# Kernel optimization log

Hardware: AMD Instinct MI355X
Metric: run time of the kernel (lower is better)

## Reference

```python
import jax, jax.numpy as jnp
import numpy as np

B, D_IN = 8192, 4096
H1, H2, LAT = 2048, 1024, 256
NQ, NL = 16, 2


def setup_inputs() -> dict:
    key = jax.random.key(0)
    ks = jax.random.split(key, 16)
    def lin(k, fan_in, fan_out):
        k1, k2 = jax.random.split(k)
        s = 1.0 / np.sqrt(fan_in)
        W = jax.random.uniform(k1, (fan_out, fan_in), jnp.float32, -s, s)
        b = jax.random.uniform(k2, (fan_out,), jnp.float32, -s, s)
        return W, b
    x = jax.random.normal(ks[0], (B, D_IN), jnp.float32)
    We1, be1 = lin(ks[1], D_IN, H1)
    We2, be2 = lin(ks[2], H1, H2)
    We3, be3 = lin(ks[3], H2, LAT)
    P = jax.random.normal(ks[4], (NL, NQ, 3), jnp.float32)  # ansatz params (rx,ry,rz)
    Wd1, bd1 = lin(ks[5], NQ, H2)
    Wd2, bd2 = lin(ks[6], H2, H1)
    Wd3, bd3 = lin(ks[7], H1, D_IN)
    return {"x": x, "We1": We1, "be1": be1, "We2": We2, "be2": be2,
            "We3": We3, "be3": be3, "P": P, "Wd1": Wd1, "bd1": bd1,
            "Wd2": Wd2, "bd2": bd2, "Wd3": Wd3, "bd3": bd3}


def _quantum_block(latent, P):
    """Exact simulation of the per-qubit circuit (all gates single-qubit, so the
    2^n statevector factorizes into per-qubit 2-vectors (a,b) over |0>,|1>).
    latent: (B, LAT), P: (NL, NQ, 3). Returns Z-expectations (B, NQ)."""
    nq = P.shape[1]
    th = latent[:, :nq]  # encoding RY angles, (B, NQ)
    # RY(th)|0> = cos(th/2)|0> + sin(th/2)|1>
    a = jnp.cos(th / 2).astype(jnp.complex64)  # (B, NQ)
    b = jnp.sin(th / 2).astype(jnp.complex64)
    for l in range(P.shape[0]):
        # RX
        t = P[l, :, 0] / 2
        c, s = jnp.cos(t).astype(jnp.complex64), jnp.sin(t).astype(jnp.complex64)
        a, b = c * a - 1j * s * b, -1j * s * a + c * b
        # RY
        t = P[l, :, 1] / 2
        c, s = jnp.cos(t).astype(jnp.complex64), jnp.sin(t).astype(jnp.complex64)
        a, b = c * a - s * b, s * a + c * b
        # RZ
        t = P[l, :, 2] / 2
        ph = jnp.exp(-1j * t.astype(jnp.complex64))
        a, b = a * ph, b * jnp.conj(ph)
    z = (a.real ** 2 + a.imag ** 2) - (b.real ** 2 + b.imag ** 2)
    return z.astype(latent.dtype)


def reference(x, We1, be1, We2, be2, We3, be3, P,
              Wd1, bd1, Wd2, bd2, Wd3, bd3):
    h = jax.nn.relu(x @ We1.T + be1)
    h = jax.nn.relu(h @ We2.T + be2)
    latent = h @ We3.T + be3            # (B, LAT)
    refined = _quantum_block(latent, P)  # (B, NQ)
    h = jax.nn.relu(refined @ Wd1.T + bd1)
    h = jax.nn.relu(h @ Wd2.T + bd2)
    return h @ Wd3.T + bd3              # (B, D_IN)
```

## Files before the change

### kernel.cpp

```cpp
#include <hip/hip_runtime.h>

typedef __attribute__((ext_vector_type(8))) short bf16x8;
typedef __attribute__((ext_vector_type(4))) float f32x4;

__device__ __forceinline__ unsigned short f2bf(float f) {
    union { float f; unsigned int u; } v; v.f = f;
    unsigned int u = v.u;
    unsigned int r = (u + 0x7FFFu + ((u >> 16) & 1u)) >> 16;
    return (unsigned short)r;
}
__device__ __forceinline__ float bf2f(unsigned short b) {
    union { unsigned int u; float f; } v; v.u = ((unsigned int)b) << 16;
    return v.f;
}

#define GL16(g, l)                                                             \
    __builtin_amdgcn_global_load_lds(                                          \
        (__attribute__((address_space(1))) void*)(void*)(g),                   \
        (__attribute__((address_space(3))) void*)(void*)(l), 16, 0, 0)

#define BAR()   __builtin_amdgcn_s_barrier()
#define LGKM0() asm volatile("s_waitcnt lgkmcnt(0)" ::: "memory")

struct Cast5 {
    const float *s0, *s1, *s2, *s3, *s4;
    unsigned short *d0, *d1, *d2, *d3, *d4;
    int n0, n1, n2, n3, total;
};
__global__ void castall(Cast5 a) {
    int stride = gridDim.x * blockDim.x;
    for (int i = blockIdx.x * blockDim.x + threadIdx.x; i < a.total; i += stride) {
        int j = i; const float* s; unsigned short* d;
        if (j < a.n0) { s = a.s0; d = a.d0; }
        else { j -= a.n0;
            if (j < a.n1) { s = a.s1; d = a.d1; }
            else { j -= a.n1;
                if (j < a.n2) { s = a.s2; d = a.d2; }
                else { j -= a.n2;
                    if (j < a.n3) { s = a.s3; d = a.d3; }
                    else { j -= a.n3; s = a.s4; d = a.d4; } } } }
        float4 v = ((const float4*)s)[j];
        ushort4 o;
        o.x = f2bf(v.x); o.y = f2bf(v.y); o.z = f2bf(v.z); o.w = f2bf(v.w);
        ((ushort4*)d)[j] = o;
    }
}


template<int RELU, int OUT_BF16, int MP>
__global__ __launch_bounds__(512, 2) void gemm8p(
    const unsigned short* __restrict__ A,
    const unsigned short* __restrict__ Bm,
    const float* __restrict__ bias,
    void* __restrict__ Cout,
    int N, int K, int NT)
{
    constexpr int AHU  = MP * 2048;
    constexpr int BOFF = MP * 8192;
    __shared__ __align__(16) unsigned short lds[MP * 8192 + 32768];

    const int tid  = threadIdx.x;
    const int lane = tid & 63;
    const int w    = tid >> 6;
    const int wm   = w >> 2;
    const int wn   = w & 3;
    const int bm   = blockIdx.x;
    const int bn   = blockIdx.y;

    const unsigned short* gA = A  + (long)bm * (MP * 64) * K;
    const unsigned short* gB = Bm + (long)bn * 256 * K;

    const int sr0 = tid >> 3;
    const int so0 = (((tid & 7) * 16) ^ ((sr0 & 7) << 4)) >> 1;
    const int loff = (sr0 * K + so0) * 2;
    const int ch1  = K * 128;
    const int lb0 = (w * 64) * 8;
    const int lb1 = (512 + w * 64) * 8;

    const int cl  = lane & 15;
    const int g16 = (lane >> 4) * 16;
    const int sw  = (cl & 7) << 4;
    const int cK0 = (g16 ^ sw) >> 1;
    const int cK1 = ((64 + g16) ^ sw) >> 1;
    const int arb = wm * (MP * 16) + cl;
    const int brb = wn * 32 + cl;
    const int aIdx0 = (arb * 64 + cK0) * 2;
    const int aIdx1 = (arb * 64 + cK1) * 2;
    const int bIdx0 = (BOFF + brb * 64 + cK0) * 2;
    const int bIdx1 = (BOFF + brb * 64 + cK1) * 2;

    f32x4  acc[2][2][MP][2] = {};
    bf16x8 a0[MP][2], a1[MP][2], bA[2][2], bB[2][2], b1[2][2];

#define GLA_(SP, DI) do {                                                      \
        GL16((const char*)(SP) + loff, &lds[0] + (DI) + lb0);                  \
        if constexpr (MP == 4) {                                               \
            GL16((const char*)(SP) + loff + ch1, &lds[0] + (DI) + lb1); }      \
    } while (0)
#define GLB_(SP, DI) do {                                                      \
        GL16((const char*)(SP) + loff, &lds[0] + (DI) + lb0);                  \
        GL16((const char*)(SP) + loff + ch1, &lds[0] + (DI) + lb1);            \
    } while (0)

#define READA_(AR, MH, PAR) do {                                               \
        _Pragma("unroll") for (int mp_ = 0; mp_ < MP; ++mp_) {                 \
            AR[mp_][0] = *(const bf16x8*)((const char*)lds + aIdx0 +           \
                         (((PAR)*2+(MH))*AHU*2 + mp_*2048));                   \
            AR[mp_][1] = *(const bf16x8*)((const char*)lds + aIdx1 +           \
                         (((PAR)*2+(MH))*AHU*2 + mp_*2048));                   \
        } } while (0)
#define READB_(BR, NH, PAR) do {                                               \
        _Pragma("unroll") for (int np_ = 0; np_ < 2; ++np_) {                  \
            BR[np_][0] = *(const bf16x8*)((const char*)lds + bIdx0 +           \
                         (((PAR)*2+(NH))*16384 + np_*2048));                   \
            BR[np_][1] = *(const bf16x8*)((const char*)lds + bIdx1 +           \
                         (((PAR)*2+(NH))*16384 + np_*2048));                   \
        } } while (0)
#define QUAD(mh, nh, AR, BR) do {                                              \
        __builtin_amdgcn_s_setprio(1);                                         \
        _Pragma("unroll") for (int kk_ = 0; kk_ < 2; ++kk_)                    \
        _Pragma("unroll") for (int mp_ = 0; mp_ < MP; ++mp_)                   \
        _Pragma("unroll") for (int np_ = 0; np_ < 2; ++np_)                    \
            acc[mh][nh][mp_][np_] = __builtin_amdgcn_mfma_f32_16x16x32_bf16(   \
                AR[mp_][kk_], BR[np_][kk_], acc[mh][nh][mp_][np_], 0, 0, 0);   \
        __builtin_amdgcn_s_setprio(0);                                         \
    } while (0)
#define VMW() do {                                                             \
        if constexpr (MP == 4) asm volatile("s_waitcnt vmcnt(6)" ::: "memory");\
        else                   asm volatile("s_waitcnt vmcnt(5)" ::: "memory");\
    } while (0)

    GLB_(gB,                      BOFF + 0);
    GLA_(gA,                      0);
    GLB_(gB + (long)128 * K,      BOFF + 8192);
    GLA_(gA + (long)(MP*32) * K,  AHU);
    GLB_(gB + 64,                 BOFF + 2*8192);
    GLA_(gA + 64,                 2*AHU);
    GLB_(gB + (long)128 * K + 64, BOFF + 3*8192);
    VMW();
    BAR();
    READA_(a0, 0, 0);
    READB_(bA, 0, 0);

    const unsigned short* sA1 = gA + (long)(MP*32) * K + 64;
    const unsigned short* sA0 = gA + 128;
    const unsigned short* sB0 = gB + 128;
    const unsigned short* sB1 = gB + (long)128 * K + 128;

#define KTILE(T, PAR, BC, BNX) do {                                            \
        const int adv1_ = ((T) + 2 < NT) ? 64 : 0;                             \
        const int adv2_ = ((T) + 3 < NT) ? 64 : 0;                             \
                                       \
        READA_(a1, 1, PAR);                                                    \
        READB_(b1, 1, PAR);                                                    \
        GLA_(sA1, (((PAR)^1)*2+1)*AHU); sA1 += adv1_;                          \
        QUAD(0, 0, a0, BC);                                                    \
                                                                       \
        GLB_(sB0, BOFF + (PAR)*2*8192); sB0 += adv2_;                          \
        VMW();                                                                 \
        BAR();                                                                 \
        QUAD(0, 1, a0, b1);                                                    \
              \
        READA_(a0, 0, (PAR)^1);                                                \
        READB_(BNX, 0, (PAR)^1);                                               \
        GLA_(sA0, (PAR)*2*AHU); sA0 += adv2_;                                  \
        QUAD(1, 1, a1, b1);                                                    \
                                                                       \
        GLB_(sB1, BOFF + ((PAR)*2+1)*8192); sB1 += adv2_;                      \
        VMW();                                                                 \
        BAR();                                                                 \
        QUAD(1, 0, a1, BC);                                                    \
    } while (0)

    for (int t = 0; t < NT; t += 2) {
        KTILE(t,     0, bA, bB);
        KTILE(t + 1, 1, bB, bA);
    }

    asm volatile("s_waitcnt vmcnt(0)" ::: "memory");
    BAR();

    const int r4 = (lane >> 4) * 4;
    float bv[2][2];
    #pragma unroll
    for (int nh = 0; nh < 2; ++nh)
        #pragma unroll
        for (int np = 0; np < 2; ++np)
            bv[nh][np] = bias[(long)bn * 256 + nh * 128 + wn * 32 + np * 16 + cl];

    if (OUT_BF16) {
        unsigned short* epi = lds;
        #pragma unroll
        for (int h = 0; h < 2; ++h) {
            if (h) { LGKM0(); BAR(); }
            #pragma unroll
            for (int mp = 0; mp < MP; ++mp)
                #pragma unroll
                for (int nh = 0; nh < 2; ++nh)
                    #pragma unroll
                    for (int np = 0; np < 2; ++np)
                        #pragma unroll
                        for (int r = 0; r < 4; ++r) {
                            float v = acc[h][nh][mp][np][r] + bv[nh][np];
                            if (RELU) v = fmaxf(v, 0.f);
                            int lrow = wm * (MP * 16) + mp * 16 + r4 + r;
                            int lcol = nh * 128 + wn * 32 + np * 16 + cl;
                            epi[lrow * 264 + lcol] = f2bf(v);
                        }
            LGKM0();
            BAR();
            long rowg0 = (long)bm * (MP * 64) + h * (MP * 32);
            #pragma unroll
            for (int i = 0; i < 2 * MP; ++i) {
                int row = (tid >> 5) + i * 16;
                int cc  = (tid & 31) * 8;
                bf16x8 v8 = *(const bf16x8*)&epi[row * 264 + cc];
                *(bf16x8*)((unsigned short*)Cout + (rowg0 + row) * (long)N + (long)bn * 256 + cc) = v8;
            }
        }
    } else {
        #pragma unroll
        for (int mh = 0; mh < 2; ++mh)
            #pragma unroll
            for (int mp = 0; mp < MP; ++mp) {
                long grow = (long)bm * (MP * 64) + mh * (MP * 32) + wm * (MP * 16) + mp * 16 + r4;
                #pragma unroll
                for (int nh = 0; nh < 2; ++nh)
                    #pragma unroll
                    for (int np = 0; np < 2; ++np) {
                        long gcol = (long)bn * 256 + nh * 128 + wn * 32 + np * 16 + cl;
                        #pragma unroll
                        for (int r = 0; r < 4; ++r) {
                            float v = acc[mh][nh][mp][np][r] + bv[nh][np];
                            if (RELU) v = fmaxf(v, 0.f);
                            ((float*)Cout)[(grow + r) * (long)N + gcol] = v;
                        }
                    }
            }
    }
#undef GLA_
#undef GLB_
#undef READA_
#undef READB_
#undef QUAD
#undef VMW
#undef KTILE
}

__global__ __launch_bounds__(256) void latq_d1(
    const unsigned short* __restrict__ h2,
    const float* __restrict__ We3,
    const float* __restrict__ be3,
    const float* __restrict__ P,
    const float* __restrict__ Wd1,
    const float* __restrict__ bd1,
    unsigned short* __restrict__ h3)
{
    __shared__ float zsh[4][16];
    const int lane = threadIdx.x & 63;
    const int wv   = threadIdx.x >> 6;
    const long row = (long)blockIdx.x * 4 + wv;

    float hreg[16];
    {
        const unsigned short* hr = h2 + row * 1024 + lane * 16;
        bf16x8 h0 = *(const bf16x8*)hr;
        bf16x8 h1v = *(const bf16x8*)(hr + 8);
        #pragma unroll
        for (int j = 0; j < 8; ++j) {
            hreg[j]     = bf2f((unsigned short)h0[j]);
            hreg[8 + j] = bf2f((unsigned short)h1v[j]);
        }
    }

    float myth = 0.f;
    #pragma unroll
    for (int q = 0; q < 16; ++q) {
        const float4* wq = (const float4*)(We3 + q * 1024 + lane * 16);
        float p = 0.f;
        #pragma unroll
        for (int c = 0; c < 4; ++c) {
            float4 w4 = wq[c];
            p += hreg[c * 4 + 0] * w4.x + hreg[c * 4 + 1] * w4.y
               + hreg[c * 4 + 2] * w4.z + hreg[c * 4 + 3] * w4.w;
        }
        #pragma unroll
        for (int o = 32; o; o >>= 1) p += __shfl_xor(p, o, 64);
        if (lane == q) myth = p + be3[q];
    }

    if (lane < 16) {
        const int q = lane;
        float ar = cosf(0.5f * myth), ai = 0.f;
        float br = sinf(0.5f * myth), bi = 0.f;
        #pragma unroll
        for (int l = 0; l < 2; ++l) {
            const float* pp = P + (l * 16 + q) * 3;
            float t, c, s, ar2, ai2, br2, bi2;
            t = 0.5f * pp[0]; c = cosf(t); s = sinf(t);
            ar2 = c * ar + s * bi;  ai2 = c * ai - s * br;
            br2 = c * br + s * ai;  bi2 = c * bi - s * ar;
            ar = ar2; ai = ai2; br = br2; bi = bi2;
            t = 0.5f * pp[1]; c = cosf(t); s = sinf(t);
            ar2 = c * ar - s * br;  ai2 = c * ai - s * bi;
            br2 = s * ar + c * br;  bi2 = s * ai + c * bi;
            ar = ar2; ai = ai2; br = br2; bi = bi2;
            t = 0.5f * pp[2]; c = cosf(t); s = sinf(t);
            ar2 = ar * c + ai * s;  ai2 = ai * c - ar * s;
            br2 = br * c - bi * s;  bi2 = bi * c + br * s;
            ar = ar2; ai = ai2; br = br2; bi = bi2;
        }
        zsh[wv][q] = ar * ar + ai * ai - (br * br + bi * bi);
    }
    __syncthreads();

    float z[16];
    #pragma unroll
    for (int q = 0; q < 16; ++q) z[q] = zsh[wv][q];

    unsigned short* orow = h3 + row * 1024;
    #pragma unroll
    for (int i = 0; i < 16; ++i) {
        int j = lane + 64 * i;
        const float4* wrow = (const float4*)(Wd1 + j * 16);
        float acc = bd1[j];
        #pragma unroll
        for (int qq = 0; qq < 4; ++qq) {
            float4 w4 = wrow[qq];
            acc += z[qq * 4 + 0] * w4.x + z[qq * 4 + 1] * w4.y
                 + z[qq * 4 + 2] * w4.z + z[qq * 4 + 3] * w4.w;
        }
        orow[j] = f2bf(fmaxf(acc, 0.f));
    }
}

extern "C" void kernel_launch(void* const* d_in, const int* in_sizes, int n_in,
                              void* d_out, int out_size, void* d_ws, size_t ws_size,
                              hipStream_t stream) {
    const float* x   = (const float*)d_in[0];
    const float* We1 = (const float*)d_in[1];
    const float* be1 = (const float*)d_in[2];
    const float* We2 = (const float*)d_in[3];
    const float* be2 = (const float*)d_in[4];
    const float* We3 = (const float*)d_in[5];
    const float* be3 = (const float*)d_in[6];
    const float* P   = (const float*)d_in[7];
    const float* Wd1 = (const float*)d_in[8];
    const float* bd1 = (const float*)d_in[9];
    const float* Wd2 = (const float*)d_in[10];
    const float* bd2 = (const float*)d_in[11];
    const float* Wd3 = (const float*)d_in[12];
    const float* bd3 = (const float*)d_in[13];

    const int B = 8192, DIN = 4096, NH1 = 2048, NH2 = 1024;

    char* w = (char*)d_ws;
    unsigned short* x_bf   = (unsigned short*)(w);
    unsigned short* h4     = x_bf;
    unsigned short* We1_bf = (unsigned short*)(w + 67108864L);
    unsigned short* We2_bf = (unsigned short*)(w + 83886080L);
    unsigned short* Wd2_bf = (unsigned short*)(w + 88080384L);
    unsigned short* Wd3_bf = (unsigned short*)(w + 92274688L);
    unsigned short* h1     = (unsigned short*)(w + 109051904L);
    unsigned short* h3     = h1;
    unsigned short* h2     = (unsigned short*)(w + 142606336L);

    Cast5 ca;
    ca.s0 = x;   ca.d0 = x_bf;   ca.n0 = (int)((long)B * DIN / 4);
    ca.s1 = We1; ca.d1 = We1_bf; ca.n1 = (int)((long)NH1 * DIN / 4);
    ca.s2 = We2; ca.d2 = We2_bf; ca.n2 = (int)((long)NH2 * NH1 / 4);
    ca.s3 = Wd2; ca.d3 = Wd2_bf; ca.n3 = (int)((long)NH1 * NH2 / 4);
    ca.s4 = Wd3; ca.d4 = Wd3_bf;
    ca.total = ca.n0 + ca.n1 + ca.n2 + ca.n3 + (int)((long)DIN * NH1 / 4);
    castall<<<2048, 256, 0, stream>>>(ca);

    gemm8p<1, 1, 4><<<dim3(B / 256, NH1 / 256), 512, 0, stream>>>(x_bf, We1_bf, be1, h1, NH1, DIN, DIN >> 6);
    gemm8p<1, 1, 2><<<dim3(B / 128, NH2 / 256), 512, 0, stream>>>(h1, We2_bf, be2, h2, NH2, NH1, NH1 >> 6);
    latq_d1<<<dim3(B / 4), 256, 0, stream>>>(h2, We3, be3, P, Wd1, bd1, h3);
    gemm8p<1, 1, 4><<<dim3(B / 256, NH1 / 256), 512, 0, stream>>>(h3, Wd2_bf, bd2, h4, NH1, NH2, NH2 >> 6);
    gemm8p<0, 0, 4><<<dim3(B / 256, DIN / 256), 512, 0, stream>>>(h4, Wd3_bf, bd3, d_out, DIN, NH1, NH1 >> 6);
}
```

Before: 391.6 us.

## Fuse fp32-to-bf16 conversion of x into the first GEMM's A-tile loads

Stops casting the 8192x4096 fp32 input to bf16 in the standalone cast kernel. The first GEMM now loads fp32 A tiles into registers, converts and packs them to bf16, and writes them to LDS itself, with lgkm waits added before the barriers. This removes a full write and re-read of the bf16 copy of x through HBM. In exchange the first GEMM reads twice the A bytes, and its A loads go through registers instead of direct global-to-LDS transfers, which adds VALU work and may weaken the load pipelining.

```diff
diff --git a/kernel.cpp b/kernel.cpp
--- a/kernel.cpp
+++ b/kernel.cpp
@@ -13,6 +13,9 @@
     union { unsigned int u; float f; } v; v.u = ((unsigned int)b) << 16;
     return v.f;
 }
+__device__ __forceinline__ unsigned int pk2bf(float lo, float hi) {
+    return ((unsigned int)f2bf(hi) << 16) | (unsigned int)f2bf(lo);
+}
 
 #define GL16(g, l)                                                             \
     __builtin_amdgcn_global_load_lds(                                          \
@@ -22,12 +25,12 @@
 #define BAR()   __builtin_amdgcn_s_barrier()
 #define LGKM0() asm volatile("s_waitcnt lgkmcnt(0)" ::: "memory")
 
-struct Cast5 {
-    const float *s0, *s1, *s2, *s3, *s4;
-    unsigned short *d0, *d1, *d2, *d3, *d4;
-    int n0, n1, n2, n3, total;
+struct Cast4 {
+    const float *s0, *s1, *s2, *s3;
+    unsigned short *d0, *d1, *d2, *d3;
+    int n0, n1, n2, total;
 };
-__global__ void castall(Cast5 a) {
+__global__ void castall(Cast4 a) {
     int stride = gridDim.x * blockDim.x;
     for (int i = blockIdx.x * blockDim.x + threadIdx.x; i < a.total; i += stride) {
         int j = i; const float* s; unsigned short* d;
@@ -36,9 +39,7 @@
             if (j < a.n1) { s = a.s1; d = a.d1; }
             else { j -= a.n1;
                 if (j < a.n2) { s = a.s2; d = a.d2; }
-                else { j -= a.n2;
-                    if (j < a.n3) { s = a.s3; d = a.d3; }
-                    else { j -= a.n3; s = a.s4; d = a.d4; } } } }
+                else { j -= a.n2; s = a.s3; d = a.d3; } } }
         float4 v = ((const float4*)s)[j];
         ushort4 o;
         o.x = f2bf(v.x); o.y = f2bf(v.y); o.z = f2bf(v.z); o.w = f2bf(v.w);
@@ -47,9 +48,9 @@
 }
 
 
-template<int RELU, int OUT_BF16, int MP>
+template<int RELU, int OUT_BF16, int MP, int AF32>
 __global__ __launch_bounds__(512, 2) void gemm8p(
-    const unsigned short* __restrict__ A,
+    const void* __restrict__ Av,
     const unsigned short* __restrict__ Bm,
     const float* __restrict__ bias,
     void* __restrict__ Cout,
@@ -58,6 +59,7 @@
     constexpr int AHU  = MP * 2048;
     constexpr int BOFF = MP * 8192;
     __shared__ __align__(16) unsigned short lds[MP * 8192 + 32768];
+    char* ldsc = (char*)lds;
 
     const int tid  = threadIdx.x;
     const int lane = tid & 63;
@@ -67,15 +69,19 @@
     const int bm   = blockIdx.x;
     const int bn   = blockIdx.y;
 
-    const unsigned short* gA = A  + (long)bm * (MP * 64) * K;
-    const unsigned short* gB = Bm + (long)bn * 256 * K;
+    const unsigned short* gA  = (const unsigned short*)Av + (long)bm * (MP * 64) * K;
+    const float*          gAf = (const float*)Av          + (long)bm * (MP * 64) * K;
+    const unsigned short* gB  = Bm + (long)bn * 256 * K;
 
     const int sr0 = tid >> 3;
     const int so0 = (((tid & 7) * 16) ^ ((sr0 & 7) << 4)) >> 1;
-    const int loff = (sr0 * K + so0) * 2;
-    const int ch1  = K * 128;
+    const int loff  = (sr0 * K + so0) * 2;
+    const int loffF = (sr0 * K + so0) * 4;
+    const int ch1   = K * 128;
+    const int ch1F  = K * 256;
     const int lb0 = (w * 64) * 8;
     const int lb1 = (512 + w * 64) * 8;
+    const int wrb = tid * 16;
 
     const int cl  = lane & 15;
     const int g16 = (lane >> 4) * 16;
@@ -90,7 +96,8 @@
     const int bIdx1 = (BOFF + brb * 64 + cK1) * 2;
 
     f32x4  acc[2][2][MP][2] = {};
-    bf16x8 a0[MP][2], a1[MP][2], bA[2][2], bB[2][2], b1[2][2];
+    bf16x8 a0[MP][2], a1[MP][2], b0[2][2], b1[2][2];
+    float4 fA0, fA1, fA2, fA3;
 
 #define GLA_(SP, DI) do {                                                      \
         GL16((const char*)(SP) + loff, &lds[0] + (DI) + lb0);                  \
@@ -100,6 +107,21 @@
 #define GLB_(SP, DI) do {                                                      \
         GL16((const char*)(SP) + loff, &lds[0] + (DI) + lb0);                  \
         GL16((const char*)(SP) + loff + ch1, &lds[0] + (DI) + lb1);            \
+    } while (0)
+#define ALD_(SPF) do {                                                         \
+        fA0 = *(const float4*)((const char*)(SPF) + loffF);                    \
+        fA1 = *(const float4*)((const char*)(SPF) + loffF + 16);               \
+        fA2 = *(const float4*)((const char*)(SPF) + loffF + ch1F);             \
+        fA3 = *(const float4*)((const char*)(SPF) + loffF + ch1F + 16);        \
+    } while (0)
+#define AWR_(DI) do {                                                          \
+        uint4 q0_, q1_;                                                        \
+        q0_.x = pk2bf(fA0.x, fA0.y); q0_.y = pk2bf(fA0.z, fA0.w);              \
+        q0_.z = pk2bf(fA1.x, fA1.y); q0_.w = pk2bf(fA1.z, fA1.w);              \
+        q1_.x = pk2bf(fA2.x, fA2.y); q1_.y = pk2bf(fA2.z, fA2.w);              \
+        q1_.z = pk2bf(fA3.x, fA3.y); q1_.w = pk2bf(fA3.z, fA3.w);              \
+        *(uint4*)(ldsc + (DI) * 2 + wrb) = q0_;                                \
+        *(uint4*)(ldsc + (DI) * 2 + 8192 + wrb) = q1_;                         \
     } while (0)
 
 #define READA_(AR, MH, PAR) do {                                               \
@@ -126,58 +148,79 @@
         __builtin_amdgcn_s_setprio(0);                                         \
     } while (0)
 #define VMW() do {                                                             \
-        if constexpr (MP == 4) asm volatile("s_waitcnt vmcnt(6)" ::: "memory");\
-        else                   asm volatile("s_waitcnt vmcnt(5)" ::: "memory");\
-    } while (0)
-
-    GLB_(gB,                      BOFF + 0);
-    GLA_(gA,                      0);
-    GLB_(gB + (long)128 * K,      BOFF + 8192);
-    GLA_(gA + (long)(MP*32) * K,  AHU);
-    GLB_(gB + 64,                 BOFF + 2*8192);
-    GLA_(gA + 64,                 2*AHU);
-    GLB_(gB + (long)128 * K + 64, BOFF + 3*8192);
+        if constexpr (AF32)        asm volatile("s_waitcnt vmcnt(4)" ::: "memory"); \
+        else if constexpr (MP == 4) asm volatile("s_waitcnt vmcnt(6)" ::: "memory");\
+        else                       asm volatile("s_waitcnt vmcnt(5)" ::: "memory");\
+    } while (0)
+#define PUB() do { if constexpr (AF32) LGKM0(); BAR(); } while (0)
+
+    if constexpr (AF32) {
+        GLB_(gB,                      BOFF + 0);
+        ALD_(gAf);                          AWR_(0);
+        GLB_(gB + (long)128 * K,      BOFF + 8192);
+        ALD_(gAf + (long)(MP*32) * K);      AWR_(AHU);
+        GLB_(gB + 64,                 BOFF + 2*8192);
+        ALD_(gAf + 64);                     AWR_(2*AHU);
+        GLB_(gB + (long)128 * K + 64, BOFF + 3*8192);
+    } else {
+        GLB_(gB,                      BOFF + 0);
+        GLA_(gA,                      0);
+        GLB_(gB + (long)128 * K,      BOFF + 8192);
+        GLA_(gA + (long)(MP*32) * K,  AHU);
+        GLB_(gB + 64,                 BOFF + 2*8192);
+        GLA_(gA + 64,                 2*AHU);
+        GLB_(gB + (long)128 * K + 64, BOFF + 3*8192);
+    }
     VMW();
-    BAR();
+    PUB();
     READA_(a0, 0, 0);
-    READB_(bA, 0, 0);
+    READB_(b0, 0, 0);
 
     const unsigned short* sA1 = gA + (long)(MP*32) * K + 64;
     const unsigned short* sA0 = gA + 128;
+    const float* sA1f = gAf + (long)(MP*32) * K + 64;
+    const float* sA0f = gAf + 128;
     const unsigned short* sB0 = gB + 128;
     const unsigned short* sB1 = gB + (long)128 * K + 128;
 
-#define KTILE(T, PAR, BC, BNX) do {                                            \
+#define KTILE(T, PAR) do {                                                     \
         const int adv1_ = ((T) + 2 < NT) ? 64 : 0;                             \
         const int adv2_ = ((T) + 3 < NT) ? 64 : 0;                             \
-                                       \
+                        \
+        if constexpr (AF32) { ALD_(sA1f); }                                    \
         READA_(a1, 1, PAR);                                                    \
         READB_(b1, 1, PAR);                                                    \
-        GLA_(sA1, (((PAR)^1)*2+1)*AHU); sA1 += adv1_;                          \
-        QUAD(0, 0, a0, BC);                                                    \
+        if constexpr (!AF32) { GLA_(sA1, (((PAR)^1)*2+1)*AHU); }               \
+        QUAD(0, 0, a0, b0);                                                    \
+        if constexpr (AF32) { AWR_((((PAR)^1)*2+1)*AHU); sA1f += adv1_; }      \
+        else                { sA1 += adv1_; }                                  \
                                                                        \
         GLB_(sB0, BOFF + (PAR)*2*8192); sB0 += adv2_;                          \
         VMW();                                                                 \
-        BAR();                                                                 \
+        PUB();                                                                 \
         QUAD(0, 1, a0, b1);                                                    \
-              \
+                             \
+        if constexpr (AF32) { ALD_(sA0f); }                                    \
         READA_(a0, 0, (PAR)^1);                                                \
-        READB_(BNX, 0, (PAR)^1);                                               \
-        GLA_(sA0, (PAR)*2*AHU); sA0 += adv2_;                                  \
+        if constexpr (!AF32) { GLA_(sA0, (PAR)*2*AHU); }                       \
         QUAD(1, 1, a1, b1);                                                    \
+        if constexpr (AF32) { AWR_((PAR)*2*AHU); sA0f += adv2_; }              \
+        else                { sA0 += adv2_; }                                  \
                                                                        \
         GLB_(sB1, BOFF + ((PAR)*2+1)*8192); sB1 += adv2_;                      \
         VMW();                                                                 \
-        BAR();                                                                 \
-        QUAD(1, 0, a1, BC);                                                    \
+        PUB();                                                                 \
+        QUAD(1, 0, a1, b0);                                                    \
+        READB_(b0, 0, (PAR)^1);      \
     } while (0)
 
     for (int t = 0; t < NT; t += 2) {
-        KTILE(t,     0, bA, bB);
-        KTILE(t + 1, 1, bB, bA);
+        KTILE(t, 0);
+        KTILE(t + 1, 1);
     }
 
     asm volatile("s_waitcnt vmcnt(0)" ::: "memory");
+    LGKM0();
     BAR();
 
     const int r4 = (lane >> 4) * 4;
@@ -240,10 +283,13 @@
     }
 #undef GLA_
 #undef GLB_
+#undef ALD_
+#undef AWR_
 #undef READA_
 #undef READB_
 #undef QUAD
 #undef VMW
+#undef PUB
 #undef KTILE
 }
 
@@ -355,8 +401,7 @@
     const int B = 8192, DIN = 4096, NH1 = 2048, NH2 = 1024;
 
     char* w = (char*)d_ws;
-    unsigned short* x_bf   = (unsigned short*)(w);
-    unsigned short* h4     = x_bf;
+    unsigned short* h4     = (unsigned short*)(w);
     unsigned short* We1_bf = (unsigned short*)(w + 67108864L);
     unsigned short* We2_bf = (unsigned short*)(w + 83886080L);
     unsigned short* Wd2_bf = (unsigned short*)(w + 88080384L);
@@ -365,18 +410,17 @@
     unsigned short* h3     = h1;
     unsigned short* h2     = (unsigned short*)(w + 142606336L);
 
-    Cast5 ca;
-    ca.s0 = x;   ca.d0 = x_bf;   ca.n0 = (int)((long)B * DIN / 4);
-    ca.s1 = We1; ca.d1 = We1_bf; ca.n1 = (int)((long)NH1 * DIN / 4);
-    ca.s2 = We2; ca.d2 = We2_bf; ca.n2 = (int)((long)NH2 * NH1 / 4);
-    ca.s3 = Wd2; ca.d3 = Wd2_bf; ca.n3 = (int)((long)NH1 * NH2 / 4);
-    ca.s4 = Wd3; ca.d4 = Wd3_bf;
-    ca.total = ca.n0 + ca.n1 + ca.n2 + ca.n3 + (int)((long)DIN * NH1 / 4);
+    Cast4 ca;
+    ca.s0 = We1; ca.d0 = We1_bf; ca.n0 = (int)((long)NH1 * DIN / 4);
+    ca.s1 = We2; ca.d1 = We2_bf; ca.n1 = (int)((long)NH2 * NH1 / 4);
+    ca.s2 = Wd2; ca.d2 = Wd2_bf; ca.n2 = (int)((long)NH1 * NH2 / 4);
+    ca.s3 = Wd3; ca.d3 = Wd3_bf;
+    ca.total = ca.n0 + ca.n1 + ca.n2 + (int)((long)DIN * NH1 / 4);
     castall<<<2048, 256, 0, stream>>>(ca);
 
-    gemm8p<1, 1, 4><<<dim3(B / 256, NH1 / 256), 512, 0, stream>>>(x_bf, We1_bf, be1, h1, NH1, DIN, DIN >> 6);
-    gemm8p<1, 1, 2><<<dim3(B / 128, NH2 / 256), 512, 0, stream>>>(h1, We2_bf, be2, h2, NH2, NH1, NH1 >> 6);
+    gemm8p<1, 1, 4, 1><<<dim3(B / 256, NH1 / 256), 512, 0, stream>>>(x, We1_bf, be1, h1, NH1, DIN, DIN >> 6);
+    gemm8p<1, 1, 2, 0><<<dim3(B / 128, NH2 / 256), 512, 0, stream>>>(h1, We2_bf, be2, h2, NH2, NH1, NH1 >> 6);
     latq_d1<<<dim3(B / 4), 256, 0, stream>>>(h2, We3, be3, P, Wd1, bd1, h3);
-    gemm8p<1, 1, 4><<<dim3(B / 256, NH1 / 256), 512, 0, stream>>>(h3, Wd2_bf, bd2, h4, NH1, NH2, NH2 >> 6);
-    gemm8p<0, 0, 4><<<dim3(B / 256, DIN / 256), 512, 0, stream>>>(h4, Wd3_bf, bd3, d_out, DIN, NH1, NH1 >> 6);
-}
+    gemm8p<1, 1, 4, 0><<<dim3(B / 256, NH1 / 256), 512, 0, stream>>>(h3, Wd2_bf, bd2, h4, NH1, NH2, NH2 >> 6);
+    gemm8p<0, 0, 4, 0><<<dim3(B / 256, DIN / 256), 512, 0, stream>>>(h4, Wd3_bf, bd3, d_out, DIN, NH1, NH1 >> 6);
+}
```

Result: slower. 525.5 us (+34.2%).
